# Kernel optimization log

Hardware: AMD Instinct MI355X
Metric: run time of the kernel (lower is better)

The kernel has to match this reference:

```python
import jax, jax.numpy as jnp
import numpy as np

B, L, D, H = 8, 512, 512, 8
E, G = 4, 2            # primary experts, ghost experts
THRESH = 0.01          # ghost_activation_threshold
EPS = 1e-5             # LayerNorm eps (torch default)


def _ln(x, s, b):
    m = x.mean(-1, keepdims=True)
    v = ((x - m) ** 2).mean(-1, keepdims=True)
    return (x - m) * jax.lax.rsqrt(v + EPS) * s + b


def _expert(x, ln1_s, ln1_b, wqkv, bqkv, wo, bo, ln2_s, ln2_b, w1, b1, w2, b2):
    # Pre-norm transformer block: MHA + residual, FFN + residual (dropout=0)
    Bn, Ln, Dn = x.shape
    dh = Dn // H
    xn = _ln(x, ln1_s, ln1_b)
    qkv = xn @ wqkv + bqkv                      # [B,L,3D]
    q, k, v = jnp.split(qkv, 3, axis=-1)
    heads = lambda t: t.reshape(Bn, Ln, H, dh).transpose(0, 2, 1, 3)
    q, k, v = heads(q), heads(k), heads(v)      # [B,H,L,dh]
    scores = jnp.einsum('bhqd,bhkd->bhqk', q, k) / np.sqrt(dh).astype(np.float32)
    attn = jax.nn.softmax(scores, axis=-1)
    o = jnp.einsum('bhqk,bhkd->bhqd', attn, v).transpose(0, 2, 1, 3).reshape(Bn, Ln, Dn)
    x = x + o @ wo + bo
    h = _ln(x, ln2_s, ln2_b)
    x = x + jax.nn.gelu(h @ w1 + b1) @ w2 + b2
    return x


def _make_params(key, n, d):
    ks = jax.random.split(key, 4)
    s = 0.02
    return dict(
        ln1_s=jnp.ones((n, d)), ln1_b=jnp.zeros((n, d)),
        wqkv=jax.random.normal(ks[0], (n, d, 3 * d)) * s, bqkv=jnp.zeros((n, 3 * d)),
        wo=jax.random.normal(ks[1], (n, d, d)) * s, bo=jnp.zeros((n, d)),
        ln2_s=jnp.ones((n, d)), ln2_b=jnp.zeros((n, d)),
        w1=jax.random.normal(ks[2], (n, d, 4 * d)) * s, b1=jnp.zeros((n, 4 * d)),
        w2=jax.random.normal(ks[3], (n, 4 * d, d)) * s, b2=jnp.zeros((n, d)))


def setup_inputs() -> dict:
    key = jax.random.key(0)
    k1, k2, k3 = jax.random.split(key, 3)
    inp = {'x': jax.random.normal(k1, (B, L, D), jnp.float32), 'step': 100}
    for pre, n, k in (('p_', E, k2), ('g_', G, k3)):
        for name, arr in _make_params(k, n, D).items():
            inp[pre + name] = arr
    return inp


def reference(x, step,
              p_ln1_s, p_ln1_b, p_wqkv, p_bqkv, p_wo, p_bo, p_ln2_s, p_ln2_b, p_w1, p_b1, p_w2, p_b2,
              g_ln1_s, g_ln1_b, g_wqkv, g_bqkv, g_wo, g_bo, g_ln2_s, g_ln2_b, g_w1, g_b1, g_w2, g_b2):
    pp = (p_ln1_s, p_ln1_b, p_wqkv, p_bqkv, p_wo, p_bo, p_ln2_s, p_ln2_b, p_w1, p_b1, p_w2, p_b2)
    gp = (g_ln1_s, g_ln1_b, g_wqkv, g_bqkv, g_wo, g_bo, g_ln2_s, g_ln2_b, g_w1, g_b1, g_w2, g_b2)
    run = jax.vmap(lambda ps: _expert(x, *ps))
    prim = run(pp)                               # [E,B,L,D]
    # --- saturation metrics (statistics only; detached like .item() in torch) ---
    mean_eo = prim.mean(axis=(1, 2))             # [E,D]
    nrm = mean_eo / jnp.linalg.norm(mean_eo, axis=1, keepdims=True)
    gram = nrm @ nrm.T                           # [E,E]
    ortho = 1.0 - jnp.mean((gram - jnp.eye(E, dtype=gram.dtype)) ** 2)
    recon = prim.mean(axis=0)                    # [B,L,D]
    uvar = jnp.var(x - recon, ddof=1)            # torch.var unbiased default
    sat = jax.lax.stop_gradient(ortho * uvar)
    # --- ghost activation (initial state: all dormant -> ghost 0 gets 0.01) ---
    base = jnp.zeros((G,), x.dtype).at[0].set(0.01)
    rates = jnp.where(sat > THRESH, base, jnp.zeros((G,), x.dtype))
    ghost = jax.vmap(lambda ps: _expert(x, *ps))(gp) * rates[:, None, None, None]  # [G,B,L,D]
    # combine: mean over all (primary + ghost) expert outputs
    out = jnp.concatenate([prim, ghost], axis=0).mean(axis=0)  # [B,L,D]
    return out
```

## Files before the change

### kernel.cpp

```cpp
#include <hip/hip_runtime.h>

typedef __bf16 bf16;
typedef __bf16 bf16x8 __attribute__((ext_vector_type(8)));
typedef float  f32x4  __attribute__((ext_vector_type(4)));
typedef float  f32x16 __attribute__((ext_vector_type(16)));

#define AS1 __attribute__((address_space(1)))
#define AS3 __attribute__((address_space(3)))

__device__ __forceinline__ void async16(const void* g, void* l) {
  __builtin_amdgcn_global_load_lds((const AS1 unsigned int*)g, (AS3 unsigned int*)l, 16, 0, 0);
}

__device__ __forceinline__ float gelu_fast(float u) {
  float z = 0.7978845608028654f * (u + 0.044715f * u * u * u);
  z = fminf(fmaxf(z, -15.f), 15.f);
  float t = __expf(2.f * z);
  return u * t / (t + 1.f);
}

template <int FOLD>
__global__ __launch_bounds__(256) void transpose_cvt(
    const float* pbase, const float* gbase, bf16* dst, int K, int M,
    const float* lnsP, const float* lnbP, const float* lnsG, const float* lnbG,
    const float* b0P, const float* b0G, float* bias_eff) {
  __shared__ float tile[32][33];
  const int z = blockIdx.z;
  const float* src = (z < 4) ? pbase + (size_t)z * K * M : gbase;
  bf16* d = dst + (size_t)z * M * K;
  const int mBlk = blockIdx.x * 32, kBlk = blockIdx.y * 32;
  const int tx = threadIdx.x, ty = threadIdx.y;
  for (int i = 0; i < 4; i++)
    tile[ty + i * 8][tx] = src[(size_t)(kBlk + ty + i * 8) * M + mBlk + tx];
  __syncthreads();
  if constexpr (FOLD) {
    const float* s  = (z < 4) ? lnsP + (size_t)z * 512 : lnsG;
    const float* bb = (z < 4) ? lnbP + (size_t)z * 512 : lnbG;
    const float sk = s[kBlk + tx];
    for (int i = 0; i < 4; i++)
      d[(size_t)(mBlk + ty + i * 8) * K + kBlk + tx] = (bf16)(tile[tx][ty + i * 8] * sk);
    if (ty == 0) {
      float acc = 0.f;
      for (int kk = 0; kk < 32; kk++) acc += bb[kBlk + kk] * tile[kk][tx];
      if (kBlk == 0) {
        const float* b0 = (z < 4) ? b0P + (size_t)z * M : b0G;
        acc += b0[mBlk + tx];
      }
      atomicAdd(&bias_eff[(size_t)z * M + mBlk + tx], acc);
    }
  } else {
    for (int i = 0; i < 4; i++)
      d[(size_t)(mBlk + ty + i * 8) * K + kBlk + tx] = (bf16)tile[tx][ty + i * 8];
  }
}

__global__ __launch_bounds__(256) void ln_plain(const float* x, bf16* out) {
  const int t = blockIdx.x, tid = threadIdx.x;
  const float* xr = x + (size_t)t * 512;
  float v0 = xr[tid], v1 = xr[tid + 256];
  float s1 = v0 + v1, s2 = v0 * v0 + v1 * v1;
  for (int off = 32; off > 0; off >>= 1) { s1 += __shfl_down(s1, off); s2 += __shfl_down(s2, off); }
  __shared__ float red[8];
  __shared__ float mv[2];
  if ((tid & 63) == 0) { red[tid >> 6] = s1; red[4 + (tid >> 6)] = s2; }
  __syncthreads();
  if (tid == 0) {
    float a = red[0] + red[1] + red[2] + red[3];
    float b = red[4] + red[5] + red[6] + red[7];
    float mean = a * (1.f / 512.f);
    float var = b * (1.f / 512.f) - mean * mean;
    mv[0] = mean; mv[1] = 1.f / sqrtf(var + 1e-5f);
  }
  __syncthreads();
  const float mean = mv[0], rs = mv[1];
  bf16* o = out + (size_t)t * 512;
  o[tid]       = (bf16)((v0 - mean) * rs);
  o[tid + 256] = (bf16)((v1 - mean) * rs);
}

__global__ __launch_bounds__(256) void ln2_kernel(const bf16* in, const float* sP, const float* bP,
                                                  const float* sG, const float* bG, bf16* out) {
  const int t = blockIdx.x, z = blockIdx.y, tid = threadIdx.x;
  const bf16* xr = in + (size_t)z * 4096 * 512 + (size_t)t * 512;
  float v0 = (float)xr[tid], v1 = (float)xr[tid + 256];
  float s1 = v0 + v1, s2 = v0 * v0 + v1 * v1;
  for (int off = 32; off > 0; off >>= 1) { s1 += __shfl_down(s1, off); s2 += __shfl_down(s2, off); }
  __shared__ float red[8];
  __shared__ float mv[2];
  if ((tid & 63) == 0) { red[tid >> 6] = s1; red[4 + (tid >> 6)] = s2; }
  __syncthreads();
  if (tid == 0) {
    float a = red[0] + red[1] + red[2] + red[3];
    float b = red[4] + red[5] + red[6] + red[7];
    float mean = a * (1.f / 512.f);
    float var = b * (1.f / 512.f) - mean * mean;
    mv[0] = mean; mv[1] = 1.f / sqrtf(var + 1e-5f);
  }
  __syncthreads();
  const float mean = mv[0], rs = mv[1];
  const float* sc = (z < 4) ? sP + (size_t)z * 512 : sG;
  const float* bi = (z < 4) ? bP + (size_t)z * 512 : bG;
  bf16* o = out + (size_t)z * 4096 * 512 + (size_t)t * 512;
  o[tid]       = (bf16)((v0 - mean) * rs * sc[tid] + bi[tid]);
  o[tid + 256] = (bf16)((v1 - mean) * rs * sc[tid + 256] + bi[tid + 256]);
}

template <int MODE>
__global__ __launch_bounds__(256, 4) void gemm_bt(
    const bf16* Abase, long long aStrideZ, const bf16* Wt,
    const float* biasP, const float* biasG, int K, int M,
    bf16* out, const void* resid, long long residStrideZ) {
  const int z = blockIdx.z;
  const int id = blockIdx.x + gridDim.x * blockIdx.y;
  const int W = gridDim.x, band = id / (W * 4), within = id % (W * 4);
  const int by = band * 4 + (within & 3), bx = within >> 2;
  const bf16* A = Abase + (size_t)z * aStrideZ;
  const bf16* B = Wt + (size_t)z * M * K;
  const float* bias = (z < 4) ? biasP + (size_t)z * M : biasG;
  __shared__ bf16 smem[128 * 136];
  bf16* As = smem;
  bf16* Bs = smem + 128 * 64;
  const int tid = threadIdx.x, wave = tid >> 6, l = tid & 63;
  const int l31 = l & 31, lh = l >> 5;
  const int wm = wave & 1, wn = wave >> 1;
  f32x16 acc[2][2];
  for (int i = 0; i < 2; i++) for (int j = 0; j < 2; j++)
    for (int r = 0; r < 16; r++) acc[i][j][r] = 0.f;
  const int rowA0 = by * 128, rowB0 = bx * 128;

  const int r0 = tid >> 3, kb0 = tid & 7;
  const bf16* ap[4];
  const bf16* bp[4];
  for (int i = 0; i < 4; i++) {
    int r = i * 32 + r0;
    int cs = (kb0 ^ ((r ^ (r >> 3)) & 7)) << 3;
    ap[i] = A + (size_t)(rowA0 + r) * K + cs;
    bp[i] = B + (size_t)(rowB0 + r) * K + cs;
  }
  int aoff[4][2], boff[4][2];
  for (int ks = 0; ks < 4; ks++) {
    for (int ti = 0; ti < 2; ti++) {
      int r = wm * 64 + ti * 32 + l31;
      aoff[ks][ti] = r * 64 + (((ks * 2 + lh) ^ ((r ^ (r >> 3)) & 7)) << 3);
    }
    for (int ni = 0; ni < 2; ni++) {
      int r = wn * 64 + ni * 32 + l31;
      boff[ks][ni] = r * 64 + (((ks * 2 + lh) ^ ((r ^ (r >> 3)) & 7)) << 3);
    }
  }

  for (int kt = 0; kt < K; kt += 64) {
    __syncthreads();
    for (int i = 0; i < 4; i++) {
      async16(ap[i] + kt, &As[(i * 256 + wave * 64) * 8]);
      async16(bp[i] + kt, &Bs[(i * 256 + wave * 64) * 8]);
    }
    __syncthreads();
    for (int ks = 0; ks < 4; ks++) {
      bf16x8 af[2], bfr[2];
      for (int ti = 0; ti < 2; ti++) af[ti] = *(const bf16x8*)&As[aoff[ks][ti]];
      for (int ni = 0; ni < 2; ni++) bfr[ni] = *(const bf16x8*)&Bs[boff[ks][ni]];
      for (int ti = 0; ti < 2; ti++)
        for (int ni = 0; ni < 2; ni++)
          acc[ti][ni] = __builtin_amdgcn_mfma_f32_32x32x16_bf16(af[ti], bfr[ni], acc[ti][ni], 0, 0, 0);
    }
  }

  __syncthreads();
  for (int ti = 0; ti < 2; ti++)
    for (int ni = 0; ni < 2; ni++) {
      int coll = wn * 64 + ni * 32 + l31;
      float bb = bias[rowB0 + coll];
      for (int reg = 0; reg < 16; reg++) {
        int row = wm * 64 + ti * 32 + (reg & 3) + 8 * (reg >> 2) + 4 * lh;
        float v = acc[ti][ni][reg] + bb;
        if constexpr (MODE == 2) v = gelu_fast(v);
        smem[row * 136 + coll] = (bf16)v;
      }
    }
  __syncthreads();
  bf16* ob = out + (size_t)z * 4096 * M;
  for (int p = 0; p < 8; p++) {
    int r = p * 16 + (tid >> 4), c0 = (tid & 15) * 8;
    bf16x8 vv = *(const bf16x8*)&smem[r * 136 + c0];
    if constexpr (MODE == 1) {
      const float* rx = (const float*)resid + (size_t)(rowA0 + r) * 512 + rowB0 + c0;
      for (int j = 0; j < 8; j++) vv[j] = (bf16)((float)vv[j] + rx[j]);
    } else if constexpr (MODE == 3) {
      const bf16* rx = (const bf16*)resid + (size_t)z * residStrideZ + (size_t)(rowA0 + r) * 512 + rowB0 + c0;
      bf16x8 rv = *(const bf16x8*)rx;
      for (int j = 0; j < 8; j++) vv[j] = (bf16)((float)vv[j] + (float)rv[j]);
    }
    *(bf16x8*)&ob[(size_t)(rowA0 + r) * M + rowB0 + c0] = vv;
  }
}

__global__ __launch_bounds__(256, 2) void attn_kernel(const bf16* qkv, bf16* o) {
  const int qt = blockIdx.x >> 6, bh = blockIdx.x & 63, z = blockIdx.y;
  const int b = bh >> 3, h = bh & 7;
  const bf16* base = qkv + (size_t)z * 4096 * 1536 + (size_t)b * 512 * 1536;
  __shared__ bf16 smem[30208];
  bf16* Vt = smem + 16384;
  bf16* Q_area = smem + 16384;
  const int tid = threadIdx.x, wave = tid >> 6, l = tid & 63;
  const int m16 = l & 15, q4 = l >> 4;
  bf16* pw = smem + 20992 + wave * 32 * 72;
  f32x4 zero4 = {0.f, 0.f, 0.f, 0.f};

  for (int i = 0; i < 4; i++) {
    int s = i * 256 + tid, r = s >> 3, kb = s & 7;
    async16(base + (size_t)(qt * 128 + r) * 1536 + h * 64 + ((kb ^ (r & 7)) << 3),
            &Q_area[(i * 256 + wave * 64) * 8]);
  }
  for (int i = 0; i < 2; i++) {
    int s = i * 256 + tid, r = s >> 3, kb = s & 7;
    async16(base + (size_t)r * 1536 + 512 + h * 64 + ((kb ^ (r & 7)) << 3),
            &smem[(i * 256 + wave * 64) * 8]);
    async16(base + (size_t)r * 1536 + 1024 + h * 64 + (kb << 3),
            &smem[8192 + (i * 256 + wave * 64) * 8]);
  }
  f32x4 Oacc[2][4];
  float l_run[2][4];
  for (int rt = 0; rt < 2; rt++)
    for (int cr = 0; cr < 4; cr++) l_run[rt][cr] = 0.f;
  for (int rt = 0; rt < 2; rt++) for (int dt = 0; dt < 4; dt++) Oacc[rt][dt] = zero4;
  __syncthreads();
  bf16x8 qf[2][2];
  for (int rt = 0; rt < 2; rt++)
    for (int ks = 0; ks < 2; ks++) {
      int r = wave * 32 + rt * 16 + m16, kb = ks * 4 + q4;
      bf16x8 q8 = *(const bf16x8*)&Q_area[r * 64 + ((kb ^ (r & 7)) << 3)];
      for (int j = 0; j < 8; j++) q8[j] = (bf16)((float)q8[j] * 0.125f);
      qf[rt][ks] = q8;
    }
  __syncthreads();

  for (int kt = 0; kt < 8; kt++) {
    const int cur = kt & 1, nxt = cur ^ 1;
    bf16* Ks = smem + cur * 4096;
    bf16* Vs = smem + 8192 + cur * 4096;
    bf16* Ksn = smem + nxt * 4096;
    bf16* Vsn = smem + 8192 + nxt * 4096;
    if (kt > 0) __syncthreads();
    if (kt < 7) {
      for (int i = 0; i < 2; i++) {
        int s = i * 256 + tid, r = s >> 3, kb = s & 7;
        async16(base + (size_t)((kt + 1) * 64 + r) * 1536 + 512 + h * 64 + ((kb ^ (r & 7)) << 3),
                &Ksn[(i * 256 + wave * 64) * 8]);
        async16(base + (size_t)((kt + 1) * 64 + r) * 1536 + 1024 + h * 64 + (kb << 3),
                &Vsn[(i * 256 + wave * 64) * 8]);
      }
    }
    {
      int d = tid & 63, kb2 = (tid >> 6) * 16;
      for (int g = 0; g < 2; g++) {
        int kbase = kb2 + g * 8;
        bf16 tmp[8];
        for (int j = 0; j < 8; j++) tmp[j] = Vs[(kbase + j) * 64 + d];
        *(bf16x8*)&Vt[d * 72 + kbase] = *(const bf16x8*)tmp;
      }
    }
    f32x4 S[2][4];
    for (int rt = 0; rt < 2; rt++)
      for (int ct = 0; ct < 4; ct++) {
        f32x4 a = zero4;
        for (int ks = 0; ks < 2; ks++) {
          int n = ct * 16 + m16, kb = (ks * 4 + q4) ^ (n & 7);
          bf16x8 kf = *(const bf16x8*)&Ks[n * 64 + (kb << 3)];
          a = __builtin_amdgcn_mfma_f32_16x16x32_bf16(qf[rt][ks], kf, a, 0, 0, 0);
        }
        S[rt][ct] = a;
      }
    for (int rt = 0; rt < 2; rt++)
      for (int cr = 0; cr < 4; cr++) {
        float rs = 0.f;
        for (int ct = 0; ct < 4; ct++) {
          float p = __expf(S[rt][ct][cr]);
          S[rt][ct][cr] = p; rs += p;
        }
        rs += __shfl_xor(rs, 1); rs += __shfl_xor(rs, 2);
        rs += __shfl_xor(rs, 4); rs += __shfl_xor(rs, 8);
        l_run[rt][cr] += rs;
      }
    for (int rt = 0; rt < 2; rt++)
      for (int ct = 0; ct < 4; ct++)
        for (int cr = 0; cr < 4; cr++)
          pw[(rt * 16 + q4 * 4 + cr) * 72 + ct * 16 + m16] = (bf16)S[rt][ct][cr];
    __syncthreads();
    for (int rt = 0; rt < 2; rt++)
      for (int dt = 0; dt < 4; dt++) {
        f32x4 a = Oacc[rt][dt];
        for (int ks = 0; ks < 2; ks++) {
          bf16x8 pf = *(const bf16x8*)&pw[(rt * 16 + m16) * 72 + ks * 32 + q4 * 8];
          bf16x8 vf = *(const bf16x8*)&Vt[(dt * 16 + m16) * 72 + ks * 32 + q4 * 8];
          a = __builtin_amdgcn_mfma_f32_16x16x32_bf16(pf, vf, a, 0, 0, 0);
        }
        Oacc[rt][dt] = a;
      }
  }
  bf16* ob = o + (size_t)z * 4096 * 512 + (size_t)(b * 512 + qt * 128 + wave * 32) * 512 + h * 64;
  for (int rt = 0; rt < 2; rt++)
    for (int dt = 0; dt < 4; dt++)
      for (int cr = 0; cr < 4; cr++) {
        int r = rt * 16 + q4 * 4 + cr;
        ob[(size_t)r * 512 + dt * 16 + m16] = (bf16)(Oacc[rt][dt][cr] / l_run[rt][cr]);
      }
}

__global__ __launch_bounds__(256) void stats_k(const bf16* eout, const float* x,
                                               float* prim_sum, float* mean_acc, float* accum) {
  const int r0 = blockIdx.x * 32;
  const int tid = threadIdx.x;
  const int c0 = tid * 2;
  float cs[4][2] = {{0.f,0.f},{0.f,0.f},{0.f,0.f},{0.f,0.f}};
  float sd = 0.f, sd2 = 0.f;
  for (int rr = 0; rr < 32; rr++) {
    int row = r0 + rr;
    float s0 = 0.f, s1 = 0.f;
    for (int e = 0; e < 4; e++) {
      const bf16* p = &eout[((size_t)e * 4096 + row) * 512 + c0];
      float f0 = (float)p[0], f1 = (float)p[1];
      cs[e][0] += f0; cs[e][1] += f1;
      s0 += f0; s1 += f1;
    }
    prim_sum[(size_t)row * 512 + c0]     = s0;
    prim_sum[(size_t)row * 512 + c0 + 1] = s1;
    float d0 = x[(size_t)row * 512 + c0]     - s0 * 0.25f;
    float d1 = x[(size_t)row * 512 + c0 + 1] - s1 * 0.25f;
    sd += d0 + d1; sd2 += d0 * d0 + d1 * d1;
  }
  for (int e = 0; e < 4; e++) {
    atomicAdd(&mean_acc[e * 512 + c0],     cs[e][0]);
    atomicAdd(&mean_acc[e * 512 + c0 + 1], cs[e][1]);
  }
  for (int off = 32; off > 0; off >>= 1) { sd += __shfl_down(sd, off); sd2 += __shfl_down(sd2, off); }
  __shared__ float r1[4], r2[4];
  if ((tid & 63) == 0) { r1[tid >> 6] = sd; r2[tid >> 6] = sd2; }
  __syncthreads();
  if (tid == 0) {
    atomicAdd(&accum[0], r1[0] + r1[1] + r1[2] + r1[3]);
    atomicAdd(&accum[1], r2[0] + r2[1] + r2[2] + r2[3]);
  }
}

__global__ void finalize_k(const float* mean_acc, const float* accum, float* rate) {
  const int l = threadIdx.x;
  float me[4][8];
  for (int e = 0; e < 4; e++)
    for (int j = 0; j < 8; j++) me[e][j] = mean_acc[e * 512 + l * 8 + j] * (1.f / 4096.f);
  float dot[4][4];
  for (int e = 0; e < 4; e++)
    for (int f = e; f < 4; f++) {
      float d = 0.f;
      for (int j = 0; j < 8; j++) d += me[e][j] * me[f][j];
      for (int off = 32; off > 0; off >>= 1) d += __shfl_xor(d, off);
      dot[e][f] = d; dot[f][e] = d;
    }
  float nrm[4];
  for (int e = 0; e < 4; e++) nrm[e] = sqrtf(dot[e][e]);
  float acc = 0.f;
  for (int e = 0; e < 4; e++)
    for (int f = 0; f < 4; f++) {
      float g = dot[e][f] / (nrm[e] * nrm[f]) - (e == f ? 1.f : 0.f);
      acc += g * g;
    }
  float ortho = 1.f - acc * (1.f / 16.f);
  float n = 2097152.f;
  float uvar = (accum[1] - accum[0] * accum[0] / n) / (n - 1.f);
  float sat = ortho * uvar;
  if (l == 0) rate[0] = (sat > 0.01f) ? 0.01f : 0.f;
}

__global__ __launch_bounds__(256) void combine_k(const float* prim, const bf16* ghost,
                                                 const float* rate, float* out) {
  float r = rate[0];
  int i = blockIdx.x * 256 + threadIdx.x;
  f32x4 p = ((const f32x4*)prim)[i];
  const bf16* g = ghost + (size_t)i * 4;
  f32x4 o;
  for (int j = 0; j < 4; j++) o[j] = (p[j] + r * (float)g[j]) * (1.f / 6.f);
  ((f32x4*)out)[i] = o;
}

extern "C" void kernel_launch(void* const* d_in, const int* in_sizes, int n_in,
                              void* d_out, int out_size, void* d_ws, size_t ws_size,
                              hipStream_t stream) {
  const float* x       = (const float*)d_in[0];
  const float* p_ln1_s = (const float*)d_in[2];
  const float* p_ln1_b = (const float*)d_in[3];
  const float* p_wqkv  = (const float*)d_in[4];
  const float* p_bqkv  = (const float*)d_in[5];
  const float* p_wo    = (const float*)d_in[6];
  const float* p_bo    = (const float*)d_in[7];
  const float* p_ln2_s = (const float*)d_in[8];
  const float* p_ln2_b = (const float*)d_in[9];
  const float* p_w1    = (const float*)d_in[10];
  const float* p_b1    = (const float*)d_in[11];
  const float* p_w2    = (const float*)d_in[12];
  const float* p_b2    = (const float*)d_in[13];
  const float* g_ln1_s = (const float*)d_in[14];
  const float* g_ln1_b = (const float*)d_in[15];
  const float* g_wqkv  = (const float*)d_in[16];
  const float* g_bqkv  = (const float*)d_in[17];
  const float* g_wo    = (const float*)d_in[18];
  const float* g_bo    = (const float*)d_in[19];
  const float* g_ln2_s = (const float*)d_in[20];
  const float* g_ln2_b = (const float*)d_in[21];
  const float* g_w1    = (const float*)d_in[22];
  const float* g_b1    = (const float*)d_in[23];
  const float* g_w2    = (const float*)d_in[24];
  const float* g_b2    = (const float*)d_in[25];

  char* ws = (char*)d_ws;
  size_t off = 0;
  auto alloc = [&](size_t bytes) { void* p = ws + off; off += (bytes + 255) & ~(size_t)255; return p; };
  bf16* wt_qkv   = (bf16*)alloc(5ull * 1536 * 512 * 2);
  bf16* wt_wo    = (bf16*)alloc(5ull * 512 * 512 * 2);
  bf16* wt_w1    = (bf16*)alloc(5ull * 2048 * 512 * 2);
  bf16* wt_w2    = (bf16*)alloc(5ull * 512 * 2048 * 2);
  bf16* xn       = (bf16*)alloc(4096ull * 512 * 2);
  bf16* act_a    = (bf16*)alloc(5ull * 4096 * 512 * 2);
  bf16* big      = (bf16*)alloc(5ull * 4096 * 2048 * 2);
  bf16* x1       = (bf16*)alloc(5ull * 4096 * 512 * 2);
  bf16* eout     = (bf16*)alloc(5ull * 4096 * 512 * 2);
  float* prim_sum = (float*)alloc(4096ull * 512 * 4);
  float* bias_eff = (float*)alloc(5ull * 1536 * 4);
  float* mean_acc = (float*)alloc(4 * 512 * 4);
  float* accum    = (float*)alloc(256);

  (void)hipMemsetAsync(bias_eff, 0, 5ull * 1536 * 4, stream);
  (void)hipMemsetAsync(mean_acc, 0, 4 * 512 * 4, stream);
  (void)hipMemsetAsync(accum, 0, 16, stream);

  dim3 tb(32, 8);
  transpose_cvt<1><<<dim3(48, 16, 5), tb, 0, stream>>>(p_wqkv, g_wqkv, wt_qkv, 512, 1536,
      p_ln1_s, p_ln1_b, g_ln1_s, g_ln1_b, p_bqkv, g_bqkv, bias_eff);
  transpose_cvt<0><<<dim3(16, 16, 5), tb, 0, stream>>>(p_wo, g_wo, wt_wo, 512, 512,
      nullptr, nullptr, nullptr, nullptr, nullptr, nullptr, nullptr);
  transpose_cvt<0><<<dim3(64, 16, 5), tb, 0, stream>>>(p_w1, g_w1, wt_w1, 512, 2048,
      nullptr, nullptr, nullptr, nullptr, nullptr, nullptr, nullptr);
  transpose_cvt<0><<<dim3(16, 64, 5), tb, 0, stream>>>(p_w2, g_w2, wt_w2, 2048, 512,
      nullptr, nullptr, nullptr, nullptr, nullptr, nullptr, nullptr);

  ln_plain<<<dim3(4096), 256, 0, stream>>>(x, xn);
  gemm_bt<0><<<dim3(12, 32, 5), 256, 0, stream>>>(xn, 0, wt_qkv, bias_eff, bias_eff + 4ull * 1536,
                                                  512, 1536, big, nullptr, 0);
  attn_kernel<<<dim3(256, 5), 256, 0, stream>>>(big, act_a);
  gemm_bt<1><<<dim3(4, 32, 5), 256, 0, stream>>>(act_a, 4096ll * 512, wt_wo, p_bo, g_bo,
                                                 512, 512, x1, x, 0);
  ln2_kernel<<<dim3(4096, 5), 256, 0, stream>>>(x1, p_ln2_s, p_ln2_b, g_ln2_s, g_ln2_b, act_a);
  gemm_bt<2><<<dim3(16, 32, 5), 256, 0, stream>>>(act_a, 4096ll * 512, wt_w1, p_b1, g_b1,
                                                  512, 2048, big, nullptr, 0);
  gemm_bt<3><<<dim3(4, 32, 5), 256, 0, stream>>>(big, 4096ll * 2048, wt_w2, p_b2, g_b2,
                                                 2048, 512, eout, x1, 4096ll * 512);
  stats_k<<<dim3(128), 256, 0, stream>>>(eout, x, prim_sum, mean_acc, accum);
  finalize_k<<<1, 64, 0, stream>>>(mean_acc, accum, accum + 2);
  combine_k<<<dim3(2048), 256, 0, stream>>>(prim_sum, eout + 4ull * 4096 * 512, accum + 2, (float*)d_out);
}
```

Baseline: 470.9 us.

## Pre-pack weights into MFMA fragment layout and load B directly to registers

```diff
diff --git a/kernel.cpp b/kernel.cpp
--- a/kernel.cpp
+++ b/kernel.cpp
@@ -17,6 +17,11 @@
   z = fminf(fmaxf(z, -15.f), 15.f);
   float t = __expf(2.f * z);
   return u * t / (t + 1.f);
+}
+
+__device__ __forceinline__ size_t pidx(int m, int k, int K) {
+  int nb = m >> 5, kk = k >> 4, l = (m & 31) + (((k >> 3) & 1) << 5), j = k & 7;
+  return (((size_t)nb * (K >> 4) + kk) * 64 + l) * 8 + j;
 }
 
 template <int FOLD>
@@ -37,8 +42,10 @@
     const float* s  = (z < 4) ? lnsP + (size_t)z * 512 : lnsG;
     const float* bb = (z < 4) ? lnbP + (size_t)z * 512 : lnbG;
     const float sk = s[kBlk + tx];
-    for (int i = 0; i < 4; i++)
-      d[(size_t)(mBlk + ty + i * 8) * K + kBlk + tx] = (bf16)(tile[tx][ty + i * 8] * sk);
+    for (int i = 0; i < 4; i++) {
+      int m = mBlk + ty + i * 8, k = kBlk + tx;
+      d[pidx(m, k, K)] = (bf16)(tile[tx][ty + i * 8] * sk);
+    }
     if (ty == 0) {
       float acc = 0.f;
       for (int kk = 0; kk < 32; kk++) acc += bb[kBlk + kk] * tile[kk][tx];
@@ -49,8 +56,10 @@
       atomicAdd(&bias_eff[(size_t)z * M + mBlk + tx], acc);
     }
   } else {
-    for (int i = 0; i < 4; i++)
-      d[(size_t)(mBlk + ty + i * 8) * K + kBlk + tx] = (bf16)tile[tx][ty + i * 8];
+    for (int i = 0; i < 4; i++) {
+      int m = mBlk + ty + i * 8, k = kBlk + tx;
+      d[pidx(m, k, K)] = (bf16)tile[tx][ty + i * 8];
+    }
   }
 }
 
@@ -115,11 +124,10 @@
   const int W = gridDim.x, band = id / (W * 4), within = id % (W * 4);
   const int by = band * 4 + (within & 3), bx = within >> 2;
   const bf16* A = Abase + (size_t)z * aStrideZ;
-  const bf16* B = Wt + (size_t)z * M * K;
+  const bf16* Bp = Wt + (size_t)z * M * K;
   const float* bias = (z < 4) ? biasP + (size_t)z * M : biasG;
-  __shared__ bf16 smem[128 * 136];
+  __shared__ bf16 smem[8704];
   bf16* As = smem;
-  bf16* Bs = smem + 128 * 64;
   const int tid = threadIdx.x, wave = tid >> 6, l = tid & 63;
   const int l31 = l & 31, lh = l >> 5;
   const int wm = wave & 1, wn = wave >> 1;
@@ -127,71 +135,77 @@
   for (int i = 0; i < 2; i++) for (int j = 0; j < 2; j++)
     for (int r = 0; r < 16; r++) acc[i][j][r] = 0.f;
   const int rowA0 = by * 128, rowB0 = bx * 128;
+  const int Kd16 = K >> 4;
+  const int nb0 = (rowB0 >> 5) + wn * 2;
 
   const int r0 = tid >> 3, kb0 = tid & 7;
   const bf16* ap[4];
-  const bf16* bp[4];
   for (int i = 0; i < 4; i++) {
     int r = i * 32 + r0;
     int cs = (kb0 ^ ((r ^ (r >> 3)) & 7)) << 3;
     ap[i] = A + (size_t)(rowA0 + r) * K + cs;
-    bp[i] = B + (size_t)(rowB0 + r) * K + cs;
-  }
-  int aoff[4][2], boff[4][2];
-  for (int ks = 0; ks < 4; ks++) {
+  }
+  int aoff[4][2];
+  for (int ks = 0; ks < 4; ks++)
     for (int ti = 0; ti < 2; ti++) {
       int r = wm * 64 + ti * 32 + l31;
       aoff[ks][ti] = r * 64 + (((ks * 2 + lh) ^ ((r ^ (r >> 3)) & 7)) << 3);
     }
-    for (int ni = 0; ni < 2; ni++) {
-      int r = wn * 64 + ni * 32 + l31;
-      boff[ks][ni] = r * 64 + (((ks * 2 + lh) ^ ((r ^ (r >> 3)) & 7)) << 3);
-    }
-  }
 
   for (int kt = 0; kt < K; kt += 64) {
     __syncthreads();
-    for (int i = 0; i < 4; i++) {
+    for (int i = 0; i < 4; i++)
       async16(ap[i] + kt, &As[(i * 256 + wave * 64) * 8]);
-      async16(bp[i] + kt, &Bs[(i * 256 + wave * 64) * 8]);
+    bf16x8 bq[2][4];
+    for (int ni = 0; ni < 2; ni++) {
+      const bf16* pp = Bp + (((size_t)(nb0 + ni) * Kd16 + (kt >> 4)) * 64 + l) * 8;
+      bq[ni][0] = *(const bf16x8*)(pp);
+      bq[ni][1] = *(const bf16x8*)(pp + 512);
+      bq[ni][2] = *(const bf16x8*)(pp + 1024);
+      bq[ni][3] = *(const bf16x8*)(pp + 1536);
     }
     __syncthreads();
     for (int ks = 0; ks < 4; ks++) {
-      bf16x8 af[2], bfr[2];
+      bf16x8 af[2];
       for (int ti = 0; ti < 2; ti++) af[ti] = *(const bf16x8*)&As[aoff[ks][ti]];
-      for (int ni = 0; ni < 2; ni++) bfr[ni] = *(const bf16x8*)&Bs[boff[ks][ni]];
       for (int ti = 0; ti < 2; ti++)
         for (int ni = 0; ni < 2; ni++)
-          acc[ti][ni] = __builtin_amdgcn_mfma_f32_32x32x16_bf16(af[ti], bfr[ni], acc[ti][ni], 0, 0, 0);
-    }
-  }
-
-  __syncthreads();
-  for (int ti = 0; ti < 2; ti++)
-    for (int ni = 0; ni < 2; ni++) {
-      int coll = wn * 64 + ni * 32 + l31;
-      float bb = bias[rowB0 + coll];
-      for (int reg = 0; reg < 16; reg++) {
-        int row = wm * 64 + ti * 32 + (reg & 3) + 8 * (reg >> 2) + 4 * lh;
-        float v = acc[ti][ni][reg] + bb;
-        if constexpr (MODE == 2) v = gelu_fast(v);
-        smem[row * 136 + coll] = (bf16)v;
-      }
-    }
+          acc[ti][ni] = __builtin_amdgcn_mfma_f32_32x32x16_bf16(af[ti], bq[ni][ks], acc[ti][ni], 0, 0, 0);
+    }
+  }
+
   __syncthreads();
   bf16* ob = out + (size_t)z * 4096 * M;
-  for (int p = 0; p < 8; p++) {
-    int r = p * 16 + (tid >> 4), c0 = (tid & 15) * 8;
-    bf16x8 vv = *(const bf16x8*)&smem[r * 136 + c0];
-    if constexpr (MODE == 1) {
-      const float* rx = (const float*)resid + (size_t)(rowA0 + r) * 512 + rowB0 + c0;
-      for (int j = 0; j < 8; j++) vv[j] = (bf16)((float)vv[j] + rx[j]);
-    } else if constexpr (MODE == 3) {
-      const bf16* rx = (const bf16*)resid + (size_t)z * residStrideZ + (size_t)(rowA0 + r) * 512 + rowB0 + c0;
-      bf16x8 rv = *(const bf16x8*)rx;
-      for (int j = 0; j < 8; j++) vv[j] = (bf16)((float)vv[j] + (float)rv[j]);
-    }
-    *(bf16x8*)&ob[(size_t)(rowA0 + r) * M + rowB0 + c0] = vv;
+  for (int p2 = 0; p2 < 2; p2++) {
+    if (wm == p2) {
+      for (int ti = 0; ti < 2; ti++)
+        for (int ni = 0; ni < 2; ni++) {
+          int coll = wn * 64 + ni * 32 + l31;
+          float bb = bias[rowB0 + coll];
+          for (int reg = 0; reg < 16; reg++) {
+            int row = ti * 32 + (reg & 3) + 8 * (reg >> 2) + 4 * lh;
+            float v = acc[ti][ni][reg] + bb;
+            if constexpr (MODE == 2) v = gelu_fast(v);
+            smem[row * 136 + coll] = (bf16)v;
+          }
+        }
+    }
+    __syncthreads();
+    for (int p = 0; p < 4; p++) {
+      int r = p * 16 + (tid >> 4), c0 = (tid & 15) * 8;
+      int grow = rowA0 + p2 * 64 + r;
+      bf16x8 vv = *(const bf16x8*)&smem[r * 136 + c0];
+      if constexpr (MODE == 1) {
+        const float* rx = (const float*)resid + (size_t)grow * 512 + rowB0 + c0;
+        for (int j = 0; j < 8; j++) vv[j] = (bf16)((float)vv[j] + rx[j]);
+      } else if constexpr (MODE == 3) {
+        const bf16* rx = (const bf16*)resid + (size_t)z * residStrideZ + (size_t)grow * 512 + rowB0 + c0;
+        bf16x8 rv = *(const bf16x8*)rx;
+        for (int j = 0; j < 8; j++) vv[j] = (bf16)((float)vv[j] + (float)rv[j]);
+      }
+      *(bf16x8*)&ob[(size_t)grow * M + rowB0 + c0] = vv;
+    }
+    if (p2 == 0) __syncthreads();
   }
 }
 
```

Result: slower. 484.6 us (+2.9%).
